# Kernel optimization log

Measured on AMD Instinct MI355X. Metric: run time of the kernel, lower is better.

Reference implementation:

```python
import jax, jax.numpy as jnp
import numpy as np

D_MODEL = 1024
NUM_HEADS = 16
D_K = D_MODEL // NUM_HEADS
SCALE = 1.0 / np.sqrt(D_K).astype(np.float32)


def _rope_cos_sin(T, d_k):
    inv_freq = 1.0 / (10000.0 ** (jnp.arange(0, d_k, 2, dtype=jnp.float32) / d_k))
    t = jnp.arange(T, dtype=jnp.float32)
    freqs = jnp.outer(t, inv_freq)                      # [T, d_k/2]
    emb = jnp.concatenate([freqs, freqs], axis=-1)      # [T, d_k]
    return jnp.cos(emb)[None, None], jnp.sin(emb)[None, None]  # [1,1,T,d_k]


def _rotate_half(x):
    x1, x2 = x[..., : x.shape[-1] // 2], x[..., x.shape[-1] // 2 :]
    return jnp.concatenate([-x2, x1], axis=-1)


def setup_inputs() -> dict:
    key = jax.random.key(0)
    ks = jax.random.split(key, 8)
    B, T, C = 2, 2048, D_MODEL
    x = jax.random.normal(ks[0], (B, T, C), dtype=jnp.float32)
    # torch nn.Linear weights are [out, in]; forward does x @ W.T
    s = 1.0 / np.sqrt(C)
    Wq = jax.random.uniform(ks[1], (C, C), jnp.float32, -s, s)
    Wk = jax.random.uniform(ks[2], (C, C), jnp.float32, -s, s)
    Wv = jax.random.uniform(ks[3], (C, C), jnp.float32, -s, s)
    Wo = jax.random.uniform(ks[4], (C, C), jnp.float32, -s, s)
    bo = jax.random.uniform(ks[5], (C,), jnp.float32, -s, s)
    sector_bias = jnp.zeros((1, NUM_HEADS, 1, 1), dtype=jnp.float32)
    sector_weights = jax.random.uniform(ks[6], (B, T), jnp.float32, 0.5, 1.5)
    # causal mask, broadcastable to [B,H,T,T]; 0 -> masked
    mask = jnp.tril(jnp.ones((T, T), dtype=jnp.int32))[None, None]
    return {
        "x": x, "Wq": Wq, "Wk": Wk, "Wv": Wv, "Wo": Wo, "bo": bo,
        "sector_bias": sector_bias, "sector_weights": sector_weights,
        "mask": mask,
    }


def reference(x, Wq, Wk, Wv, Wo, bo, sector_bias, sector_weights, mask):
    B, T, C = x.shape
    H, dk = NUM_HEADS, D_K
    q = (x @ Wq.T).reshape(B, T, H, dk).transpose(0, 2, 1, 3)  # [B,H,T,dk]
    k = (x @ Wk.T).reshape(B, T, H, dk).transpose(0, 2, 1, 3)
    v = (x @ Wv.T).reshape(B, T, H, dk).transpose(0, 2, 1, 3)
    cos, sin = _rope_cos_sin(T, dk)
    q = q * cos + _rotate_half(q) * sin
    k = k * cos + _rotate_half(k) * sin
    scores = jnp.einsum("bhqd,bhkd->bhqk", q, k) * SCALE
    scores = scores + sector_bias
    scores = scores * sector_weights[:, None, None, :]  # broadcast over key dim
    scores = jnp.where(mask == 0, -jnp.inf, scores)
    attn = jax.nn.softmax(scores, axis=-1)
    out = jnp.einsum("bhqk,bhkd->bhqd", attn, v)
    out = out.transpose(0, 2, 1, 3).reshape(B, T, C)
    return out @ Wo.T + bo
```

## Files before the change

kernel.cpp:

```cpp
#include <hip/hip_runtime.h>


typedef __bf16 bf16x8 __attribute__((ext_vector_type(8)));
typedef float f32x4 __attribute__((ext_vector_type(4)));
typedef float f32x16 __attribute__((ext_vector_type(16)));
typedef unsigned short u16x8 __attribute__((ext_vector_type(8)));

__device__ __forceinline__ unsigned short f2bf(float f) {
    union { float f; unsigned int u; } c; c.f = f;
    unsigned int u = c.u;
    unsigned int r = u + 0x7fffu + ((u >> 16) & 1u);
    return (unsigned short)(r >> 16);
}
__device__ __forceinline__ unsigned cvtpk(float lo, float hi) {
    unsigned r;
    asm("v_cvt_pk_bf16_f32 %0, %1, %2" : "=v"(r) : "v"(lo), "v"(hi));
    return r;
}
__device__ __forceinline__ void plswap(unsigned a, unsigned b, unsigned& r0, unsigned& r1) {
#if __has_builtin(__builtin_amdgcn_permlane32_swap)
    auto s = __builtin_amdgcn_permlane32_swap(a, b, false, false);
    r0 = (unsigned)s[0]; r1 = (unsigned)s[1];
#else
    const int hh = (int)(threadIdx.x & 63) >> 5;
    const unsigned oa = (unsigned)__shfl_xor((int)a, 32);
    const unsigned ob = (unsigned)__shfl_xor((int)b, 32);
    r0 = hh ? ob : a;
    r1 = hh ? b : oa;
#endif
}
__device__ __forceinline__ void stage8_f32(unsigned short* dst, const float* src) {
    const float4 a = *(const float4*)src;
    const float4 b = *(const float4*)(src + 4);
    u16x8 v;
    v[0] = f2bf(a.x); v[1] = f2bf(a.y); v[2] = f2bf(a.z); v[3] = f2bf(a.w);
    v[4] = f2bf(b.x); v[5] = f2bf(b.y); v[6] = f2bf(b.z); v[7] = f2bf(b.w);
    *(u16x8*)dst = v;
}
__device__ __forceinline__ void async16(const unsigned short* g, unsigned short* l) {
    __builtin_amdgcn_global_load_lds(
        (const __attribute__((address_space(1))) void*)g,
        (__attribute__((address_space(3))) void*)l, 16, 0, 0);
}

__global__ __launch_bounds__(256) void cvt_all(
    const float* __restrict__ x, const float* __restrict__ Wq, const float* __restrict__ Wk,
    const float* __restrict__ Wv, const float* __restrict__ Wo,
    unsigned short* __restrict__ dst, int hasX, int n8)
{
    const int i = blockIdx.x * 256 + threadIdx.x;
    if (i >= n8) return;
    int r = i;
    const float* src; int off;
    const int xg = hasX ? 524288 : 0;
    if (r < xg) { src = x; off = r; }
    else {
        r -= xg;
        const int w = r >> 17, o = r & 131071;
        src = (w == 0) ? Wq : (w == 1) ? Wk : (w == 2) ? Wv : Wo;
        off = o;
    }
    stage8_f32(&dst[(size_t)i * 8], &src[(size_t)off * 8]);
}

template<int A_BF16>
__global__ __launch_bounds__(256) void gemm_qkv(
    const void* __restrict__ Av, const unsigned short* __restrict__ Wb,
    unsigned short* __restrict__ outv, const float* __restrict__ swg)
{
    constexpr int K = 1024, BK = 32, NS = K / BK;
    __shared__ __align__(16) unsigned short As[3][128 * BK];
    __shared__ __align__(16) unsigned short Bs[3][128 * BK];
    const int tid = threadIdx.x;
    const int wid = tid >> 6, lane = tid & 63, g = lane >> 4, l = lane & 15;
    const int wm = (wid & 1) * 64, wn = (wid >> 1) * 64;

    const int lin = blockIdx.x + (blockIdx.y << 3) + (blockIdx.z << 8);
    const int wg  = (lin & 7) * 96 + (lin >> 3);
    const int bx = wg & 7, by = (wg >> 3) & 31, bz = wg >> 8;
    const int m0 = by * 128, n0 = bx * 128;
    const int z = bz;
    const unsigned short* W = Wb + (size_t)z * 1048576;

    f32x4 acc[4][4];
#pragma unroll
    for (int i = 0; i < 4; ++i)
#pragma unroll
        for (int j = 0; j < 4; ++j) acc[i][j] = f32x4{0.f, 0.f, 0.f, 0.f};

    const int r = tid >> 2;
    const int c = (tid & 3) * 8;

    auto stage = [&](int buf, int k0) {
        const unsigned short* A = (const unsigned short*)Av;
        unsigned short* AsW = &As[buf][wid * 512];
        async16(&A[(size_t)(m0 + r) * K + k0 + c], AsW);
        async16(&A[(size_t)(m0 + 64 + r) * K + k0 + c], AsW + 2048);
        unsigned short* BsW = &Bs[buf][wid * 512];
        async16(&W[(size_t)(n0 + r) * K + k0 + c], BsW);
        async16(&W[(size_t)(n0 + 64 + r) * K + k0 + c], BsW + 2048);
    };
    auto compute = [&](int buf) {
        const unsigned short* Asr = As[buf];
        const unsigned short* Bsr = Bs[buf];
        bf16x8 af[4], bfr[4];
#pragma unroll
        for (int im = 0; im < 4; ++im) af[im]  = *(const bf16x8*)&Asr[(wm + im * 16 + l) * BK + g * 8];
#pragma unroll
        for (int in = 0; in < 4; ++in) bfr[in] = *(const bf16x8*)&Bsr[(wn + in * 16 + l) * BK + g * 8];
#pragma unroll
        for (int im = 0; im < 4; ++im)
#pragma unroll
            for (int in = 0; in < 4; ++in)
                acc[im][in] = __builtin_amdgcn_mfma_f32_16x16x32_bf16(af[im], bfr[in], acc[im][in], 0, 0, 0);
    };

    if (A_BF16) {
        stage(0, 0);
        stage(1, BK);
        for (int ks = 0; ks < NS; ++ks) {
            if (ks + 1 < NS) asm volatile("s_waitcnt vmcnt(4)" ::: "memory");
            else             asm volatile("s_waitcnt vmcnt(0)" ::: "memory");
            __builtin_amdgcn_s_barrier();
            compute(ks % 3);
            if (ks + 2 < NS) stage((ks + 2) % 3, (ks + 2) * BK);
        }
    } else {
        auto stageF = [&](int buf, int k0) {
            const float* A = (const float*)Av;
            stage8_f32(&As[buf][tid * 8],        &A[(size_t)(m0 + r) * K + k0 + c]);
            stage8_f32(&As[buf][tid * 8 + 2048], &A[(size_t)(m0 + 64 + r) * K + k0 + c]);
            unsigned short* BsW = &Bs[buf][wid * 512];
            async16(&W[(size_t)(n0 + r) * K + k0 + c], BsW);
            async16(&W[(size_t)(n0 + 64 + r) * K + k0 + c], BsW + 2048);
        };
        stageF(0, 0);
        __syncthreads();
        for (int k0 = 0; k0 < K; k0 += BK) {
            const int cur = (k0 >> 5) & 1;
            if (k0 + BK < K) stageF(cur ^ 1, k0 + BK);
            compute(cur);
            __syncthreads();
        }
    }

    unsigned short* outq = outv + (size_t)z * 4194304;
    if (z < 2) {
        const int hq = (n0 + wn) >> 6;
        float freq[2];
#pragma unroll
        for (int in = 0; in < 2; ++in)
            freq[in] = exp2f(-(float)(in * 16 + l) * 0.41524101186f);
#pragma unroll
        for (int im = 0; im < 4; ++im)
#pragma unroll
            for (int i = 0; i < 4; ++i) {
                const int m = m0 + wm + im * 16 + g * 4 + i;
                const int b = m >> 11, t = m & 2047;
                float fw = 1.0f;
                if (z == 1) fw = 0.18033688011f * swg[(b << 11) + t];
                const size_t fq = (size_t)((b << 4) + hq) * 131072
                                + (size_t)((t >> 5) << 2) * 512
                                + (size_t)((((l >> 3) & 1) << 5) + (t & 31)) * 8 + (l & 7);
#pragma unroll
                for (int in = 0; in < 2; ++in) {
                    const float ang = (float)t * freq[in];
                    const float cs = __cosf(ang), sn = __sinf(ang);
                    const float x1 = acc[im][in][i], x2 = acc[im][in + 2][i];
                    outq[fq + (size_t)in * 512]       = f2bf((x1 * cs - x2 * sn) * fw);
                    outq[fq + (size_t)(in + 2) * 512] = f2bf((x2 * cs + x1 * sn) * fw);
                }
            }
    } else {
#pragma unroll
        for (int im = 0; im < 4; ++im)
#pragma unroll
            for (int in = 0; in < 4; ++in) {
                const int n = n0 + wn + in * 16 + l;
                const int h = n >> 6, d = n & 63;
                const int mb = m0 + wm + im * 16 + g * 4;
                const int bq = mb >> 11, t0 = mb & 2047;
                ushort4 pk;
                pk.x = f2bf(acc[im][in][0]); pk.y = f2bf(acc[im][in][1]);
                pk.z = f2bf(acc[im][in][2]); pk.w = f2bf(acc[im][in][3]);
                const size_t fv = (size_t)((bq << 4) + h) * 131072
                                + (size_t)(((t0 >> 5) << 2) + ((d >> 5) << 1) + ((t0 >> 4) & 1)) * 512
                                + (size_t)((((t0 >> 3) & 1) << 5) + (d & 31)) * 8 + (t0 & 7);
                *(ushort4*)&outq[fv] = pk;
            }
    }
}

__global__ __launch_bounds__(256) void gemm_proj(
    const unsigned short* __restrict__ A, const unsigned short* __restrict__ W,
    float* __restrict__ out, const float* __restrict__ bias)
{
    constexpr int K = 1024, BK = 32, NS = K / BK;
    __shared__ __align__(16) unsigned short As[3][64 * BK];
    __shared__ __align__(16) unsigned short Bs[3][128 * BK];
    const int tid = threadIdx.x;
    const int wid = tid >> 6, lane = tid & 63, g = lane >> 4, l = lane & 15;
    const int wm = (wid & 1) * 32, wn = (wid >> 1) * 64;

    const int lin = blockIdx.x + (blockIdx.y << 3);
    const int wg  = (lin & 7) * 64 + (lin >> 3);
    const int m0 = (wg >> 3) * 64, n0 = (wg & 7) * 128;

    f32x4 acc[2][4];
#pragma unroll
    for (int i = 0; i < 2; ++i)
#pragma unroll
        for (int j = 0; j < 4; ++j) acc[i][j] = f32x4{0.f, 0.f, 0.f, 0.f};

    const int r = tid >> 2;
    const int c = (tid & 3) * 8;

    auto stage = [&](int buf, int k0) {
        unsigned short* AsW = &As[buf][wid * 512];
        unsigned short* BsW = &Bs[buf][wid * 512];
        async16(&A[(size_t)(m0 + r) * K + k0 + c], AsW);
        async16(&W[(size_t)(n0 + r) * K + k0 + c], BsW);
        async16(&W[(size_t)(n0 + 64 + r) * K + k0 + c], BsW + 2048);
    };

    stage(0, 0);
    stage(1, BK);
    for (int ks = 0; ks < NS; ++ks) {
        if (ks + 1 < NS) asm volatile("s_waitcnt vmcnt(3)" ::: "memory");
        else             asm volatile("s_waitcnt vmcnt(0)" ::: "memory");
        __builtin_amdgcn_s_barrier();
        const unsigned short* Asr = As[ks % 3];
        const unsigned short* Bsr = Bs[ks % 3];
        bf16x8 af[2], bfr[4];
#pragma unroll
        for (int im = 0; im < 2; ++im) af[im]  = *(const bf16x8*)&Asr[(wm + im * 16 + l) * BK + g * 8];
#pragma unroll
        for (int in = 0; in < 4; ++in) bfr[in] = *(const bf16x8*)&Bsr[(wn + in * 16 + l) * BK + g * 8];
#pragma unroll
        for (int im = 0; im < 2; ++im)
#pragma unroll
            for (int in = 0; in < 4; ++in)
                acc[im][in] = __builtin_amdgcn_mfma_f32_16x16x32_bf16(af[im], bfr[in], acc[im][in], 0, 0, 0);
        if (ks + 2 < NS) stage((ks + 2) % 3, (ks + 2) * BK);
    }

#pragma unroll
    for (int im = 0; im < 2; ++im)
#pragma unroll
        for (int in = 0; in < 4; ++in) {
            const int n = n0 + wn + in * 16 + l;
#pragma unroll
            for (int i = 0; i < 4; ++i) {
                const int m = m0 + wm + im * 16 + g * 4 + i;
                out[(size_t)m * 1024 + n] = acc[im][in][i] + bias[n];
            }
        }
}

__global__ __launch_bounds__(128, 2) void flash_attn(
    const unsigned short* __restrict__ Qf, const unsigned short* __restrict__ Kf,
    const unsigned short* __restrict__ Vf, const float* __restrict__ sbias,
    const float* __restrict__ sw, unsigned short* __restrict__ attn)
{
    constexpr int T = 2048;
    __shared__ float Cmb[3072];

    const int tid = threadIdx.x, wid = tid >> 6, lane = tid & 63;
    const int hl = lane & 31, hh = lane >> 5;
    const int id = blockIdx.x;
    const int p  = 63 - (id >> 5);
    const int bh = id & 31, b = bh >> 4, h = bh & 15;
    const size_t fb = (size_t)bh * 131072;
    const float bias = sbias[h];
    const float* swb = sw + b * T;

    bf16x8 onef;
#pragma unroll
    for (int j = 0; j < 8; ++j) onef[j] = (__bf16)1.0f;

    const int q0 = p * 32;
    bf16x8 qf[4];
#pragma unroll
    for (int ks = 0; ks < 4; ++ks)
        qf[ks] = *(const bf16x8*)&Qf[fb + (size_t)(p * 4 + ks) * 512 + lane * 8];

    f32x16 oacc[2], lrow;
#pragma unroll
    for (int r = 0; r < 16; ++r) { oacc[0][r] = 0.f; oacc[1][r] = 0.f; lrow[r] = 0.f; }

    for (int c = wid; c <= p; c += 2) {
        const unsigned short* kb = &Kf[fb + (size_t)c * 2048 + lane * 8];
        const unsigned short* vb = &Vf[fb + (size_t)c * 2048 + lane * 8];

        const bf16x8 kf0 = *(const bf16x8*)&kb[0];
        const bf16x8 kf1 = *(const bf16x8*)&kb[512];
        const bf16x8 kf2 = *(const bf16x8*)&kb[1024];
        const bf16x8 kf3 = *(const bf16x8*)&kb[1536];
        f32x16 sx;
#pragma unroll
        for (int r = 0; r < 16; ++r) sx[r] = 0.f;
        sx = __builtin_amdgcn_mfma_f32_32x32x16_bf16(kf0, qf[0], sx, 0, 0, 0);
        sx = __builtin_amdgcn_mfma_f32_32x32x16_bf16(kf1, qf[1], sx, 0, 0, 0);
        sx = __builtin_amdgcn_mfma_f32_32x32x16_bf16(kf2, qf[2], sx, 0, 0, 0);
        sx = __builtin_amdgcn_mfma_f32_32x32x16_bf16(kf3, qf[3], sx, 0, 0, 0);

        const bf16x8 vf00 = *(const bf16x8*)&vb[0];
        const bf16x8 vf01 = *(const bf16x8*)&vb[512];
        const bf16x8 vf10 = *(const bf16x8*)&vb[1024];
        const bf16x8 vf11 = *(const bf16x8*)&vb[1536];

        if (bias != 0.0f) {
            const float bn = bias * 1.44269504f;
#pragma unroll
            for (int r = 0; r < 16; ++r) {
                const int kl = (r & 3) + 8 * (r >> 2) + 4 * hh;
                sx[r] += bn * swb[c * 32 + kl];
            }
        }
        if (c == p) {
#pragma unroll
            for (int r = 0; r < 16; ++r) {
                const int kl = (r & 3) + 8 * (r >> 2) + 4 * hh;
                sx[r] = (kl <= hl) ? sx[r] : -1e30f;
            }
        }
#pragma unroll
        for (int r = 0; r < 16; ++r) sx[r] = exp2f(sx[r]);

        unsigned wds[8];
#pragma unroll
        for (int g2 = 0; g2 < 4; ++g2) {
            wds[g2 * 2]     = cvtpk(sx[g2 * 4],     sx[g2 * 4 + 1]);
            wds[g2 * 2 + 1] = cvtpk(sx[g2 * 4 + 2], sx[g2 * 4 + 3]);
        }
        bf16x8 pf[2];
#pragma unroll
        for (int ks = 0; ks < 2; ++ks) {
            unsigned a0, a1, b0, b1;
            plswap(wds[4 * ks],     wds[4 * ks + 2], a0, a1);
            plswap(wds[4 * ks + 1], wds[4 * ks + 3], b0, b1);
            union { unsigned u[4]; bf16x8 v; } pk_;
            pk_.u[0] = a0; pk_.u[1] = b0;
            pk_.u[2] = a1; pk_.u[3] = b1;
            pf[ks] = pk_.v;
        }

        lrow = __builtin_amdgcn_mfma_f32_32x32x16_bf16(pf[0], onef, lrow, 0, 0, 0);
        lrow = __builtin_amdgcn_mfma_f32_32x32x16_bf16(pf[1], onef, lrow, 0, 0, 0);

        oacc[0] = __builtin_amdgcn_mfma_f32_32x32x16_bf16(pf[0], vf00, oacc[0], 0, 0, 0);
        oacc[0] = __builtin_amdgcn_mfma_f32_32x32x16_bf16(pf[1], vf01, oacc[0], 0, 0, 0);
        oacc[1] = __builtin_amdgcn_mfma_f32_32x32x16_bf16(pf[0], vf10, oacc[1], 0, 0, 0);
        oacc[1] = __builtin_amdgcn_mfma_f32_32x32x16_bf16(pf[1], vf11, oacc[1], 0, 0, 0);
    }

    __syncthreads();
    if (wid == 1) {
#pragma unroll
        for (int dt = 0; dt < 2; ++dt)
#pragma unroll
            for (int r = 0; r < 16; ++r) Cmb[(dt * 16 + r) * 64 + lane] = oacc[dt][r];
#pragma unroll
        for (int r = 0; r < 16; ++r) Cmb[2048 + r * 64 + lane] = lrow[r];
    }
    __syncthreads();
    if (wid == 0) {
#pragma unroll
        for (int r = 0; r < 16; ++r) {
            const float li = 1.0f / (lrow[r] + Cmb[2048 + r * 64 + lane]);
            const int row = (r & 3) + 8 * (r >> 2) + 4 * hh;
            const int qr = q0 + row;
#pragma unroll
            for (int dt = 0; dt < 2; ++dt) {
                const float ov = oacc[dt][r] + Cmb[(dt * 16 + r) * 64 + lane];
                attn[(size_t)(b * T + qr) * 1024 + h * 64 + dt * 32 + hl] = f2bf(ov * li);
            }
        }
    }
}

extern "C" void kernel_launch(void* const* d_in, const int* in_sizes, int n_in,
                              void* d_out, int out_size, void* d_ws, size_t ws_size,
                              hipStream_t stream) {
    const float* x  = (const float*)d_in[0];
    const float* Wq = (const float*)d_in[1];
    const float* Wk = (const float*)d_in[2];
    const float* Wv = (const float*)d_in[3];
    const float* Wo = (const float*)d_in[4];
    const float* bo = (const float*)d_in[5];
    const float* sb = (const float*)d_in[6];
    const float* sw = (const float*)d_in[7];

    const size_t QKV_SZ = 4194304;
    const size_t W_SZ   = 1048576;
    unsigned short* ws16 = (unsigned short*)d_ws;
    const bool big = ws_size >= 2 * (4 * QKV_SZ + 4 * W_SZ);

    if (big) {
        unsigned short* xb    = ws16;
        unsigned short* Wb3   = xb + QKV_SZ;
        unsigned short* Wob   = Wb3 + 3 * W_SZ;
        unsigned short* qkv   = Wob + W_SZ;
        unsigned short* attnb = xb;

        cvt_all<<<4096, 256, 0, stream>>>(x, Wq, Wk, Wv, Wo, xb, 1, 1048576);
        gemm_qkv<1><<<dim3(8, 32, 3), 256, 0, stream>>>(xb, Wb3, qkv, sw);
        flash_attn<<<2048, 128, 0, stream>>>(qkv, qkv + QKV_SZ, qkv + 2 * QKV_SZ,
                                             sb, sw, attnb);
        gemm_proj<<<dim3(8, 64), 256, 0, stream>>>(attnb, Wob, (float*)d_out, bo);
    } else {
        unsigned short* qkv   = ws16;
        unsigned short* attnb = qkv + 3 * QKV_SZ;
        unsigned short* Wb3   = attnb;
        unsigned short* Wob   = qkv;

        cvt_all<<<1536, 256, 0, stream>>>(x, Wq, Wk, Wv, Wo, Wb3, 0, 393216);
        gemm_qkv<0><<<dim3(8, 32, 3), 256, 0, stream>>>(x, Wb3, qkv, sw);
        flash_attn<<<2048, 128, 0, stream>>>(qkv, qkv + QKV_SZ, qkv + 2 * QKV_SZ,
                                             sb, sw, attnb);
        cvt_all<<<512, 256, 0, stream>>>(x, Wo, Wo, Wo, Wo, Wob, 0, 131072);
        gemm_proj<<<dim3(8, 64), 256, 0, stream>>>(attnb, Wob, (float*)d_out, bo);
    }
}
```

Baseline: 188.2 us.

## Swizzle LDS tiles and unroll triple-buffer GEMM loop by three

```diff
diff --git a/kernel.cpp b/kernel.cpp
--- a/kernel.cpp
+++ b/kernel.cpp
@@ -68,7 +68,7 @@
     const void* __restrict__ Av, const unsigned short* __restrict__ Wb,
     unsigned short* __restrict__ outv, const float* __restrict__ swg)
 {
-    constexpr int K = 1024, BK = 32, NS = K / BK;
+    constexpr int K = 1024, BK = 32;
     __shared__ __align__(16) unsigned short As[3][128 * BK];
     __shared__ __align__(16) unsigned short Bs[3][128 * BK];
     const int tid = threadIdx.x;
@@ -88,26 +88,24 @@
 #pragma unroll
         for (int j = 0; j < 4; ++j) acc[i][j] = f32x4{0.f, 0.f, 0.f, 0.f};
 
-    const int r = tid >> 2;
-    const int c = (tid & 3) * 8;
-
-    auto stage = [&](int buf, int k0) {
-        const unsigned short* A = (const unsigned short*)Av;
-        unsigned short* AsW = &As[buf][wid * 512];
-        async16(&A[(size_t)(m0 + r) * K + k0 + c], AsW);
-        async16(&A[(size_t)(m0 + 64 + r) * K + k0 + c], AsW + 2048);
-        unsigned short* BsW = &Bs[buf][wid * 512];
-        async16(&W[(size_t)(n0 + r) * K + k0 + c], BsW);
-        async16(&W[(size_t)(n0 + 64 + r) * K + k0 + c], BsW + 2048);
-    };
+    const int r  = tid >> 2;
+    const int cs = (((tid & 3) ^ ((tid >> 3) & 3)) * 8);
+    const int xg = (g ^ ((l >> 1) & 3)) * 8;
+    int aoff[4], boff[4];
+#pragma unroll
+    for (int im = 0; im < 4; ++im) aoff[im] = (wm + im * 16 + l) * BK + xg;
+#pragma unroll
+    for (int in = 0; in < 4; ++in) boff[in] = (wn + in * 16 + l) * BK + xg;
+
+    const unsigned short* Wg0 = &W[(size_t)(n0 + r) * K + cs];
+    const unsigned short* Wg1 = Wg0 + (size_t)64 * K;
+
     auto compute = [&](int buf) {
-        const unsigned short* Asr = As[buf];
-        const unsigned short* Bsr = Bs[buf];
         bf16x8 af[4], bfr[4];
 #pragma unroll
-        for (int im = 0; im < 4; ++im) af[im]  = *(const bf16x8*)&Asr[(wm + im * 16 + l) * BK + g * 8];
-#pragma unroll
-        for (int in = 0; in < 4; ++in) bfr[in] = *(const bf16x8*)&Bsr[(wn + in * 16 + l) * BK + g * 8];
+        for (int im = 0; im < 4; ++im) af[im]  = *(const bf16x8*)&As[buf][aoff[im]];
+#pragma unroll
+        for (int in = 0; in < 4; ++in) bfr[in] = *(const bf16x8*)&Bs[buf][boff[in]];
 #pragma unroll
         for (int im = 0; im < 4; ++im)
 #pragma unroll
@@ -116,23 +114,43 @@
     };
 
     if (A_BF16) {
+        const unsigned short* A = (const unsigned short*)Av;
+        const unsigned short* Ag0 = &A[(size_t)(m0 + r) * K + cs];
+        const unsigned short* Ag1 = Ag0 + (size_t)64 * K;
+        auto stage = [&](int buf, int k0) {
+            unsigned short* AsW = &As[buf][wid * 512];
+            async16(Ag0 + k0, AsW);
+            async16(Ag1 + k0, AsW + 2048);
+            unsigned short* BsW = &Bs[buf][wid * 512];
+            async16(Wg0 + k0, BsW);
+            async16(Wg1 + k0, BsW + 2048);
+        };
         stage(0, 0);
         stage(1, BK);
-        for (int ks = 0; ks < NS; ++ks) {
-            if (ks + 1 < NS) asm volatile("s_waitcnt vmcnt(4)" ::: "memory");
-            else             asm volatile("s_waitcnt vmcnt(0)" ::: "memory");
-            __builtin_amdgcn_s_barrier();
-            compute(ks % 3);
-            if (ks + 2 < NS) stage((ks + 2) % 3, (ks + 2) * BK);
-        }
+        for (int t = 0; t < 10; ++t) {
+            const int tb = t * 96;
+#pragma unroll
+            for (int u = 0; u < 3; ++u) {
+                asm volatile("s_waitcnt vmcnt(4)" ::: "memory");
+                __builtin_amdgcn_s_barrier();
+                compute(u);
+                stage((u + 2) % 3, tb + (u + 2) * BK);
+            }
+        }
+        asm volatile("s_waitcnt vmcnt(4)" ::: "memory");
+        __builtin_amdgcn_s_barrier();
+        compute(0);
+        asm volatile("s_waitcnt vmcnt(0)" ::: "memory");
+        __builtin_amdgcn_s_barrier();
+        compute(1);
     } else {
         auto stageF = [&](int buf, int k0) {
             const float* A = (const float*)Av;
-            stage8_f32(&As[buf][tid * 8],        &A[(size_t)(m0 + r) * K + k0 + c]);
-            stage8_f32(&As[buf][tid * 8 + 2048], &A[(size_t)(m0 + 64 + r) * K + k0 + c]);
+            stage8_f32(&As[buf][(tid >> 2) * BK + cs],        &A[(size_t)(m0 + r) * K + k0 + cs]);
+            stage8_f32(&As[buf][(tid >> 2) * BK + cs + 2048], &A[(size_t)(m0 + 64 + r) * K + k0 + cs]);
             unsigned short* BsW = &Bs[buf][wid * 512];
-            async16(&W[(size_t)(n0 + r) * K + k0 + c], BsW);
-            async16(&W[(size_t)(n0 + 64 + r) * K + k0 + c], BsW + 2048);
+            async16(Wg0 + k0, BsW);
+            async16(Wg1 + k0, BsW + 2048);
         };
         stageF(0, 0);
         __syncthreads();
@@ -165,10 +183,10 @@
 #pragma unroll
                 for (int in = 0; in < 2; ++in) {
                     const float ang = (float)t * freq[in];
-                    const float cs = __cosf(ang), sn = __sinf(ang);
+                    const float cs2 = __cosf(ang), sn = __sinf(ang);
                     const float x1 = acc[im][in][i], x2 = acc[im][in + 2][i];
-                    outq[fq + (size_t)in * 512]       = f2bf((x1 * cs - x2 * sn) * fw);
-                    outq[fq + (size_t)(in + 2) * 512] = f2bf((x2 * cs + x1 * sn) * fw);
+                    outq[fq + (size_t)in * 512]       = f2bf((x1 * cs2 - x2 * sn) * fw);
+                    outq[fq + (size_t)(in + 2) * 512] = f2bf((x2 * cs2 + x1 * sn) * fw);
                 }
             }
     } else {
@@ -195,7 +213,7 @@
     const unsigned short* __restrict__ A, const unsigned short* __restrict__ W,
     float* __restrict__ out, const float* __restrict__ bias)
 {
-    constexpr int K = 1024, BK = 32, NS = K / BK;
+    constexpr int K = 1024, BK = 32;
     __shared__ __align__(16) unsigned short As[3][64 * BK];
     __shared__ __align__(16) unsigned short Bs[3][128 * BK];
     const int tid = threadIdx.x;
@@ -212,37 +230,56 @@
 #pragma unroll
         for (int j = 0; j < 4; ++j) acc[i][j] = f32x4{0.f, 0.f, 0.f, 0.f};
 
-    const int r = tid >> 2;
-    const int c = (tid & 3) * 8;
+    const int r  = tid >> 2;
+    const int cs = (((tid & 3) ^ ((tid >> 3) & 3)) * 8);
+    const int xg = (g ^ ((l >> 1) & 3)) * 8;
+    int aoff[2], boff[4];
+#pragma unroll
+    for (int im = 0; im < 2; ++im) aoff[im] = (wm + im * 16 + l) * BK + xg;
+#pragma unroll
+    for (int in = 0; in < 4; ++in) boff[in] = (wn + in * 16 + l) * BK + xg;
+
+    const unsigned short* Ag0 = &A[(size_t)(m0 + r) * K + cs];
+    const unsigned short* Wg0 = &W[(size_t)(n0 + r) * K + cs];
+    const unsigned short* Wg1 = Wg0 + (size_t)64 * K;
 
     auto stage = [&](int buf, int k0) {
-        unsigned short* AsW = &As[buf][wid * 512];
+        async16(Ag0 + k0, &As[buf][wid * 512]);
         unsigned short* BsW = &Bs[buf][wid * 512];
-        async16(&A[(size_t)(m0 + r) * K + k0 + c], AsW);
-        async16(&W[(size_t)(n0 + r) * K + k0 + c], BsW);
-        async16(&W[(size_t)(n0 + 64 + r) * K + k0 + c], BsW + 2048);
+        async16(Wg0 + k0, BsW);
+        async16(Wg1 + k0, BsW + 2048);
+    };
+    auto compute = [&](int buf) {
+        bf16x8 af[2], bfr[4];
+#pragma unroll
+        for (int im = 0; im < 2; ++im) af[im]  = *(const bf16x8*)&As[buf][aoff[im]];
+#pragma unroll
+        for (int in = 0; in < 4; ++in) bfr[in] = *(const bf16x8*)&Bs[buf][boff[in]];
+#pragma unroll
+        for (int im = 0; im < 2; ++im)
+#pragma unroll
+            for (int in = 0; in < 4; ++in)
+                acc[im][in] = __builtin_amdgcn_mfma_f32_16x16x32_bf16(af[im], bfr[in], acc[im][in], 0, 0, 0);
     };
 
     stage(0, 0);
     stage(1, BK);
-    for (int ks = 0; ks < NS; ++ks) {
-        if (ks + 1 < NS) asm volatile("s_waitcnt vmcnt(3)" ::: "memory");
-        else             asm volatile("s_waitcnt vmcnt(0)" ::: "memory");
-        __builtin_amdgcn_s_barrier();
-        const unsigned short* Asr = As[ks % 3];
-        const unsigned short* Bsr = Bs[ks % 3];
-        bf16x8 af[2], bfr[4];
-#pragma unroll
-        for (int im = 0; im < 2; ++im) af[im]  = *(const bf16x8*)&Asr[(wm + im * 16 + l) * BK + g * 8];
-#pragma unroll
-        for (int in = 0; in < 4; ++in) bfr[in] = *(const bf16x8*)&Bsr[(wn + in * 16 + l) * BK + g * 8];
-#pragma unroll
-        for (int im = 0; im < 2; ++im)
-#pragma unroll
-            for (int in = 0; in < 4; ++in)
-                acc[im][in] = __builtin_amdgcn_mfma_f32_16x16x32_bf16(af[im], bfr[in], acc[im][in], 0, 0, 0);
-        if (ks + 2 < NS) stage((ks + 2) % 3, (ks + 2) * BK);
-    }
+    for (int t = 0; t < 10; ++t) {
+        const int tb = t * 96;
+#pragma unroll
+        for (int u = 0; u < 3; ++u) {
+            asm volatile("s_waitcnt vmcnt(3)" ::: "memory");
+            __builtin_amdgcn_s_barrier();
+            compute(u);
+            stage((u + 2) % 3, tb + (u + 2) * BK);
+        }
+    }
+    asm volatile("s_waitcnt vmcnt(3)" ::: "memory");
+    __builtin_amdgcn_s_barrier();
+    compute(0);
+    asm volatile("s_waitcnt vmcnt(0)" ::: "memory");
+    __builtin_amdgcn_s_barrier();
+    compute(1);
 
 #pragma unroll
     for (int im = 0; im < 2; ++im)
```

Result: no change. 191.3 us (+1.6%).
